# Kernel optimization log

Measured on AMD Instinct MI355X. Metric: run time of the kernel, lower is better.

The kernel has to match this reference:

```python
import jax, jax.numpy as jnp
import numpy as np

DIM_IN = 256  # dim_in_d * dim_in_length


def _quad_feats(h):
    # h: [B, d] -> [B, d + d*(d+1)//2] : concat(h, triu(outer(h, h)))
    d = h.shape[1]
    iu, ju = jnp.triu_indices(d)  # includes diagonal, matching torch.triu_indices
    outer = h[:, :, None] * h[:, None, :]          # [B, d, d]
    hsq = outer[:, iu, ju]                         # [B, d*(d+1)//2]
    return jnp.concatenate([h, hsq], axis=-1)


def setup_inputs() -> dict:
    key = jax.random.key(0)
    ks = jax.random.split(key, 7)
    d = DIM_IN
    q = d + (d * d + d) // 2  # 33152
    scale = 0.01  # keep activations bounded through quadratic features
    return {
        "x": jax.random.normal(ks[0], (4096, 16, 16), dtype=jnp.float32),
        "W0": jax.random.normal(ks[1], (256, q), dtype=jnp.float32) * scale,
        "b0": jax.random.normal(ks[2], (256,), dtype=jnp.float32) * scale,
        "W1": jax.random.normal(ks[3], (256, q), dtype=jnp.float32) * scale,
        "b1": jax.random.normal(ks[4], (256,), dtype=jnp.float32) * scale,
        "W2": jax.random.normal(ks[5], (10, q), dtype=jnp.float32) * scale,
        "b2": jax.random.normal(ks[6], (10,), dtype=jnp.float32) * scale,
    }


def reference(x, W0, b0, W1, b1, W2, b2):
    B = x.shape[0]
    h = x.reshape(B, -1)  # flatten: [B, dim_in_d*dim_in_length]
    for W, b in ((W0, b0), (W1, b1), (W2, b2)):
        z = _quad_feats(h)                  # [B, d + d(d+1)/2]
        h = jnp.einsum('bq,oq->bo', z, W) + b
    return h
```

## Files before the change

kernel.cpp:

```cpp
#include <hip/hip_runtime.h>
#include <stdint.h>

#define Q_IN 33152
#define NTILES 1160
#define TPC 145

typedef _Float16 half8 __attribute__((ext_vector_type(8)));
typedef float floatx4 __attribute__((ext_vector_type(4)));
typedef uint32_t uint4v __attribute__((ext_vector_type(4)));

__global__ void build_tab(uint32_t* tab) {
  int T = blockIdx.x * 256 + threadIdx.x;
  if (T >= NTILES) return;
  int kch = T / TPC, tt = T % TPC;
  int i0, jb;
  if (tt == 0) { i0 = -1; jb = 32 * kch; }
  else {
    int Q = kch * 144 + (tt - 1);
    int grp = Q >> 5, s = Q & 31;
    int g = 0, base = 0;
    for (; g < 8; ++g) { int cnt = 8 - g; if (grp < base + cnt) break; base += cnt; }
    int jt = grp - base;
    i0 = 32 * g + s;
    jb = 32 * (g + jt);
  }
  tab[T] = (((uint32_t)(uint16_t)(short)i0) << 16) | (uint32_t)(uint16_t)jb;
}

__global__ void convert_w(const float* __restrict__ W, _Float16* __restrict__ Wt,
                          const uint32_t* __restrict__ tab, int NTT, int Oreal) {
  int tid = blockIdx.x * 256 + threadIdx.x;
  if (tid >= NTILES * NTT * 64) return;
  int l = tid & 63;
  int nt = (tid >> 6) % NTT;
  int T = tid / (64 * NTT);
  int o = nt * 16 + (l & 15);
  int koff = (l >> 4) * 8;
  half8 v;
#pragma unroll
  for (int t = 0; t < 8; ++t) v[t] = (_Float16)0.f;
  if (o < Oreal) {
    uint32_t e = tab[T];
    int i0 = (short)(e >> 16);
    int jb = (int)(e & 0xFFFFu);
    const float* row = W + (size_t)o * Q_IN;
    if (i0 < 0) {
#pragma unroll
      for (int t = 0; t < 8; ++t) v[t] = (_Float16)row[jb + koff + t];
    } else {
      int qb = 256 + i0 * 256 - (i0 * (i0 - 1)) / 2 - i0;
#pragma unroll
      for (int t = 0; t < 8; ++t) {
        int j = jb + koff + t;
        if (j >= i0) v[t] = (_Float16)row[qb + j];
      }
    }
  }
  *(half8*)(Wt + (size_t)(T * NTT + nt) * 512 + l * 8) = v;
}

__global__ void reduce_h(const float* __restrict__ part, const float* __restrict__ bias,
                         float* __restrict__ h) {
  int t = blockIdx.x * 256 + threadIdx.x;
  float4 acc = *(const float4*)(bias + ((t & 63) << 2));
#pragma unroll
  for (int k = 0; k < 8; ++k) {
    float4 p = *(const float4*)(part + (size_t)k * 1048576 + t * 4);
    acc.x += p.x; acc.y += p.y; acc.z += p.z; acc.w += p.w;
  }
  *(float4*)(h + t * 4) = acc;
}

__global__ void reduce_out(const float* __restrict__ part2, const float* __restrict__ b2,
                           float* __restrict__ out) {
  int t = blockIdx.x * 256 + threadIdx.x;
  if (t >= 40960) return;
  int b = t / 10, o = t - b * 10;
  float acc = b2[o];
#pragma unroll
  for (int k = 0; k < 8; ++k) acc += part2[(size_t)k * 65536 + b * 16 + o];
  out[t] = acc;
}

__device__ inline floatx4 mfma16(half8 a, half8 b, floatx4 c) {
  return __builtin_amdgcn_mfma_f32_16x16x32_f16(a, b, c, 0, 0, 0);
}

__device__ inline half8 splat_mul_lo(half8 a, uint32_t s) {
  uint4v av = __builtin_bit_cast(uint4v, a), r;
#pragma unroll
  for (int k = 0; k < 4; ++k)
    asm("v_pk_mul_f16 %0, %1, %2 op_sel:[0,0] op_sel_hi:[1,0]"
        : "=v"(r[k]) : "v"(av[k]), "v"(s));
  return __builtin_bit_cast(half8, r);
}
__device__ inline half8 splat_mul_hi(half8 a, uint32_t s) {
  uint4v av = __builtin_bit_cast(uint4v, a), r;
#pragma unroll
  for (int k = 0; k < 4; ++k)
    asm("v_pk_mul_f16 %0, %1, %2 op_sel:[0,1] op_sel_hi:[1,1]"
        : "=v"(r[k]) : "v"(av[k]), "v"(s));
  return __builtin_bit_cast(half8, r);
}

__global__ __launch_bounds__(512, 1) void qgemm_main(
    const float* __restrict__ hIn, const _Float16* __restrict__ Wt,
    float* __restrict__ part, const uint32_t* __restrict__ gtab) {
  __shared__ _Float16 hT[128 * 256];

  const int tid = threadIdx.x;
  const int l = tid & 63;
  const int wid = tid >> 6;
  const int wm = wid >> 2;
  const int wn = wid & 3;
  const int kch = blockIdx.x & 7;
  const int rb = blockIdx.x >> 3;
  const int tbase = kch * TPC;

  const char* gb = (const char*)Wt + (size_t)tbase * 16384;
  const char* gq = gb + 16384;
  const uint32_t lo = (uint32_t)(wn * 4096 + l * 16);

  half8 blin[4];
#pragma unroll
  for (int j = 0; j < 4; ++j)
    blin[j] = *(const half8*)(gb + (lo + j * 1024u));

  half8 G0[2][4], G1[2][4];
  auto issueG0 = [&](uint32_t qt) {
#pragma unroll
    for (int t2 = 0; t2 < 2; ++t2)
#pragma unroll
      for (int j = 0; j < 4; ++j)
        G0[t2][j] = *(const half8*)(gq + (lo + (qt + t2) * 16384u + j * 1024u));
  };
  auto issueG1 = [&](uint32_t qt) {
#pragma unroll
    for (int t2 = 0; t2 < 2; ++t2)
#pragma unroll
      for (int j = 0; j < 4; ++j)
        G1[t2][j] = *(const half8*)(gq + (lo + (qt + t2) * 16384u + j * 1024u));
  };
  issueG0(0);
  issueG1(2);

  {
    int r = tid >> 2, sg = tid & 3;
    const float* src = hIn + (size_t)(rb * 128 + r) * 256 + sg * 64;
    char* dst = (char*)hT + r * 512;
    int xo = (r & 7) << 4;
#pragma unroll
    for (int oc = 0; oc < 8; ++oc) {
      float4 f0 = *(const float4*)(src + oc * 8);
      float4 f1 = *(const float4*)(src + oc * 8 + 4);
      half8 hv;
      hv[0] = (_Float16)f0.x; hv[1] = (_Float16)f0.y;
      hv[2] = (_Float16)f0.z; hv[3] = (_Float16)f0.w;
      hv[4] = (_Float16)f1.x; hv[5] = (_Float16)f1.y;
      hv[6] = (_Float16)f1.z; hv[7] = (_Float16)f1.w;
      *(half8*)(dst + ((sg * 128 + oc * 16) ^ xo)) = hv;
    }
  }
  __syncthreads();

  floatx4 acc[4][4];
#pragma unroll
  for (int mt = 0; mt < 4; ++mt)
#pragma unroll
    for (int nt = 0; nt < 4; ++nt)
#pragma unroll
      for (int rg = 0; rg < 4; ++rg) acc[mt][nt][rg] = 0.f;

  int rowb[4];
#pragma unroll
  for (int mt = 0; mt < 4; ++mt)
    rowb[mt] = (wm * 64 + mt * 16 + (l & 15)) * 512;
  const int xorb = (l & 7) << 4;
  const int koffA = (l >> 4) * 16;
  const char* hTb = (const char*)hT;

  half8 a[4];
  uint4v scu[4];
  int prevjb;

  auto loadA = [&](int jb) {
#pragma unroll
    for (int mt = 0; mt < 4; ++mt)
      a[mt] = *(const half8*)(hTb + rowb[mt] + ((jb * 2 + koffA) ^ xorb));
  };
  auto consumeG0 = [&](const int t2, const int s) {
#pragma unroll
    for (int mt = 0; mt < 4; ++mt) {
      uint32_t sd = scu[mt][s >> 1];
      half8 as_ = (s & 1) ? splat_mul_hi(a[mt], sd) : splat_mul_lo(a[mt], sd);
#pragma unroll
      for (int j = 0; j < 4; ++j)
        acc[mt][j] = mfma16(as_, G0[t2][j], acc[mt][j]);
    }
  };
  auto consumeG1 = [&](const int t2, const int s) {
#pragma unroll
    for (int mt = 0; mt < 4; ++mt) {
      uint32_t sd = scu[mt][s >> 1];
      half8 as_ = (s & 1) ? splat_mul_hi(a[mt], sd) : splat_mul_lo(a[mt], sd);
#pragma unroll
      for (int j = 0; j < 4; ++j)
        acc[mt][j] = mfma16(as_, G1[t2][j], acc[mt][j]);
    }
  };

  {
    uint32_t e0 = gtab[tbase];
    int jb = (int)(e0 & 0xFFFFu);
    loadA(jb);
#pragma unroll
    for (int mt = 0; mt < 4; ++mt)
#pragma unroll
      for (int j = 0; j < 4; ++j)
        acc[mt][j] = mfma16(a[mt], blin[j], acc[mt][j]);
    prevjb = jb;
  }

  uint32_t qt = 0;
  for (int blk = 0; blk < 18; ++blk) {
    uint32_t e = gtab[tbase + 1 + blk * 8];
    int i0b = (int)(e >> 16);
    int jb = (int)(e & 0xFFFFu);
#pragma unroll
    for (int mt = 0; mt < 4; ++mt)
      scu[mt] = *(const uint4v*)(hTb + rowb[mt] + ((i0b * 2) ^ xorb));
    if (jb != prevjb) { prevjb = jb; loadA(jb); }

    consumeG0(0, 0); consumeG0(1, 1); issueG0(qt + 4);
    consumeG1(0, 2); consumeG1(1, 3); issueG1(qt + 6);
    consumeG0(0, 4); consumeG0(1, 5); if (blk < 17) issueG0(qt + 8);
    consumeG1(0, 6); consumeG1(1, 7); if (blk < 17) issueG1(qt + 10);
    qt += 8;
  }

  float* op = part + (size_t)kch * 1048576;
#pragma unroll
  for (int mt = 0; mt < 4; ++mt) {
    int rbase = rb * 128 + wm * 64 + mt * 16 + (l >> 4) * 4;
#pragma unroll
    for (int nt = 0; nt < 4; ++nt) {
      int c = wn * 64 + nt * 16 + (l & 15);
#pragma unroll
      for (int rg = 0; rg < 4; ++rg)
        op[(size_t)(rbase + rg) * 256 + c] = acc[mt][nt][rg];
    }
  }
}

__global__ __launch_bounds__(512, 2) void qgemm_small(
    const float* __restrict__ hIn, const _Float16* __restrict__ Wt,
    float* __restrict__ part2, const uint32_t* __restrict__ gtab) {
  __shared__ _Float16 hT[128 * 256];
  const int tid = threadIdx.x;
  const int l = tid & 63;
  const int wid = tid >> 6;
  const int kch = blockIdx.x & 7;
  const int rb = blockIdx.x >> 3;
  const int tbase = kch * TPC;

  {
    int r = tid >> 2, sg = tid & 3;
    const float* src = hIn + (size_t)(rb * 128 + r) * 256 + sg * 64;
    char* dst = (char*)hT + r * 512;
    int xo = (r & 7) << 4;
#pragma unroll
    for (int oc = 0; oc < 8; ++oc) {
      float4 f0 = *(const float4*)(src + oc * 8);
      float4 f1 = *(const float4*)(src + oc * 8 + 4);
      half8 hv;
      hv[0] = (_Float16)f0.x; hv[1] = (_Float16)f0.y;
      hv[2] = (_Float16)f0.z; hv[3] = (_Float16)f0.w;
      hv[4] = (_Float16)f1.x; hv[5] = (_Float16)f1.y;
      hv[6] = (_Float16)f1.z; hv[7] = (_Float16)f1.w;
      *(half8*)(dst + ((sg * 128 + oc * 16) ^ xo)) = hv;
    }
  }
  __syncthreads();

  floatx4 acc;
#pragma unroll
  for (int rg = 0; rg < 4; ++rg) acc[rg] = 0.f;

  const int rowb = (wid * 16 + (l & 15)) * 512;
  const int xorb = (l & 7) << 4;
  const int koffA = (l >> 4) * 16;
  const char* hTb = (const char*)hT;

  half8 a, sc;
  int prevjb;

  {
    uint32_t e0 = gtab[tbase];
    int jb = (int)(e0 & 0xFFFFu);
    a = *(const half8*)(hTb + rowb + ((jb * 2 + koffA) ^ xorb));
    half8 b = *(const half8*)(Wt + (size_t)tbase * 512 + l * 8);
    acc = mfma16(a, b, acc);
    prevjb = jb;
  }

  for (int u8 = 0; u8 < 18; ++u8) {
    uint32_t e = gtab[tbase + 1 + u8 * 8];
    int i0b = (int)(e >> 16);
    int jb = (int)(e & 0xFFFFu);
    const int ttb = tbase + 1 + u8 * 8;
    half8 bq[8];
#pragma unroll
    for (int s = 0; s < 8; ++s)
      bq[s] = *(const half8*)(Wt + (size_t)(ttb + s) * 512 + l * 8);
    if (jb != prevjb) {
      prevjb = jb;
      a = *(const half8*)(hTb + rowb + ((jb * 2 + koffA) ^ xorb));
    }
    sc = *(const half8*)(hTb + rowb + ((i0b * 2) ^ xorb));
#pragma unroll
    for (int s = 0; s < 8; ++s) {
      _Float16 sv = sc[s];
      half8 sb = {sv, sv, sv, sv, sv, sv, sv, sv};
      acc = mfma16(a * sb, bq[s], acc);
    }
  }

  float* op = part2 + (size_t)kch * 65536;
  const int r0 = rb * 128 + wid * 16 + (l >> 4) * 4;
  const int c = l & 15;
#pragma unroll
  for (int rg = 0; rg < 4; ++rg)
    op[(size_t)(r0 + rg) * 16 + c] = acc[rg];
}

extern "C" void kernel_launch(void* const* d_in, const int* in_sizes, int n_in,
                              void* d_out, int out_size, void* d_ws, size_t ws_size,
                              hipStream_t stream) {
  const float* x = (const float*)d_in[0];
  const float* W0 = (const float*)d_in[1];
  const float* b0 = (const float*)d_in[2];
  const float* W1 = (const float*)d_in[3];
  const float* b1 = (const float*)d_in[4];
  const float* W2 = (const float*)d_in[5];
  const float* b2 = (const float*)d_in[6];
  float* out = (float*)d_out;

  char* ws = (char*)d_ws;
  float* h1 = (float*)ws;
  float* h2 = (float*)(ws + (4u << 20));
  _Float16* Wt = (_Float16*)(ws + (8u << 20));
  uint32_t* tab = (uint32_t*)(ws + (8u << 20) + 19005440u);
  float* part = (float*)(ws + (28u << 20));
  float* part2 = part;

  build_tab<<<(NTILES + 255) / 256, 256, 0, stream>>>(tab);

  convert_w<<<(NTILES * 16 * 64) / 256, 256, 0, stream>>>(W0, Wt, tab, 16, 256);
  qgemm_main<<<256, 512, 0, stream>>>(x, Wt, part, tab);
  reduce_h<<<1024, 256, 0, stream>>>(part, b0, h1);
  convert_w<<<(NTILES * 16 * 64) / 256, 256, 0, stream>>>(W1, Wt, tab, 16, 256);
  qgemm_main<<<256, 512, 0, stream>>>(h1, Wt, part, tab);
  reduce_h<<<1024, 256, 0, stream>>>(part, b1, h2);
  convert_w<<<(NTILES * 1 * 64 + 255) / 256, 256, 0, stream>>>(W2, Wt, tab, 1, 10);
  qgemm_small<<<256, 512, 0, stream>>>(h2, Wt, part2, tab);
  reduce_out<<<160, 256, 0, stream>>>(part2, b2, out);
}
```

Measured before the change: 249.1 us.

## Shrink weight prefetch buffers in main GEMM and split-K small GEMM further

In the main quadratic GEMM, the double-buffered weight prefetch drops from two tiles per buffer to one tile per buffer, issued after every consume step, with a peeled final block. This frees registers, possibly enough to raise occupancy or cut spills, but the prefetch distance becomes shorter. The small final-layer GEMM is split over twice as many K chunks (512 blocks instead of 256) to use more CUs, and the output reduction now sums 16 partials instead of 8.

```diff
diff --git a/kernel.cpp b/kernel.cpp
--- a/kernel.cpp
+++ b/kernel.cpp
@@ -78,7 +78,7 @@
   int b = t / 10, o = t - b * 10;
   float acc = b2[o];
 #pragma unroll
-  for (int k = 0; k < 8; ++k) acc += part2[(size_t)k * 65536 + b * 16 + o];
+  for (int k = 0; k < 16; ++k) acc += part2[(size_t)k * 65536 + b * 16 + o];
   out[t] = acc;
 }
 
@@ -126,23 +126,19 @@
   for (int j = 0; j < 4; ++j)
     blin[j] = *(const half8*)(gb + (lo + j * 1024u));
 
-  half8 G0[2][4], G1[2][4];
-  auto issueG0 = [&](uint32_t qt) {
-#pragma unroll
-    for (int t2 = 0; t2 < 2; ++t2)
-#pragma unroll
-      for (int j = 0; j < 4; ++j)
-        G0[t2][j] = *(const half8*)(gq + (lo + (qt + t2) * 16384u + j * 1024u));
-  };
-  auto issueG1 = [&](uint32_t qt) {
-#pragma unroll
-    for (int t2 = 0; t2 < 2; ++t2)
-#pragma unroll
-      for (int j = 0; j < 4; ++j)
-        G1[t2][j] = *(const half8*)(gq + (lo + (qt + t2) * 16384u + j * 1024u));
+  half8 G0[4], G1[4];
+  auto issueG0 = [&](uint32_t t) {
+#pragma unroll
+    for (int j = 0; j < 4; ++j)
+      G0[j] = *(const half8*)(gq + (lo + t * 16384u + j * 1024u));
+  };
+  auto issueG1 = [&](uint32_t t) {
+#pragma unroll
+    for (int j = 0; j < 4; ++j)
+      G1[j] = *(const half8*)(gq + (lo + t * 16384u + j * 1024u));
   };
   issueG0(0);
-  issueG1(2);
+  issueG1(1);
 
   {
     int r = tid >> 2, sg = tid & 3;
@@ -188,24 +184,24 @@
     for (int mt = 0; mt < 4; ++mt)
       a[mt] = *(const half8*)(hTb + rowb[mt] + ((jb * 2 + koffA) ^ xorb));
   };
-  auto consumeG0 = [&](const int t2, const int s) {
+  auto consume0 = [&](const int s) {
 #pragma unroll
     for (int mt = 0; mt < 4; ++mt) {
       uint32_t sd = scu[mt][s >> 1];
       half8 as_ = (s & 1) ? splat_mul_hi(a[mt], sd) : splat_mul_lo(a[mt], sd);
 #pragma unroll
       for (int j = 0; j < 4; ++j)
-        acc[mt][j] = mfma16(as_, G0[t2][j], acc[mt][j]);
-    }
-  };
-  auto consumeG1 = [&](const int t2, const int s) {
+        acc[mt][j] = mfma16(as_, G0[j], acc[mt][j]);
+    }
+  };
+  auto consume1 = [&](const int s) {
 #pragma unroll
     for (int mt = 0; mt < 4; ++mt) {
       uint32_t sd = scu[mt][s >> 1];
       half8 as_ = (s & 1) ? splat_mul_hi(a[mt], sd) : splat_mul_lo(a[mt], sd);
 #pragma unroll
       for (int j = 0; j < 4; ++j)
-        acc[mt][j] = mfma16(as_, G1[t2][j], acc[mt][j]);
+        acc[mt][j] = mfma16(as_, G1[j], acc[mt][j]);
     }
   };
 
@@ -222,7 +218,7 @@
   }
 
   uint32_t qt = 0;
-  for (int blk = 0; blk < 18; ++blk) {
+  for (int blk = 0; blk < 17; ++blk) {
     uint32_t e = gtab[tbase + 1 + blk * 8];
     int i0b = (int)(e >> 16);
     int jb = (int)(e & 0xFFFFu);
@@ -231,11 +227,33 @@
       scu[mt] = *(const uint4v*)(hTb + rowb[mt] + ((i0b * 2) ^ xorb));
     if (jb != prevjb) { prevjb = jb; loadA(jb); }
 
-    consumeG0(0, 0); consumeG0(1, 1); issueG0(qt + 4);
-    consumeG1(0, 2); consumeG1(1, 3); issueG1(qt + 6);
-    consumeG0(0, 4); consumeG0(1, 5); if (blk < 17) issueG0(qt + 8);
-    consumeG1(0, 6); consumeG1(1, 7); if (blk < 17) issueG1(qt + 10);
+    consume0(0); issueG0(qt + 2);
+    consume1(1); issueG1(qt + 3);
+    consume0(2); issueG0(qt + 4);
+    consume1(3); issueG1(qt + 5);
+    consume0(4); issueG0(qt + 6);
+    consume1(5); issueG1(qt + 7);
+    consume0(6); issueG0(qt + 8);
+    consume1(7); issueG1(qt + 9);
     qt += 8;
+  }
+  {
+    uint32_t e = gtab[tbase + 1 + 17 * 8];
+    int i0b = (int)(e >> 16);
+    int jb = (int)(e & 0xFFFFu);
+#pragma unroll
+    for (int mt = 0; mt < 4; ++mt)
+      scu[mt] = *(const uint4v*)(hTb + rowb[mt] + ((i0b * 2) ^ xorb));
+    if (jb != prevjb) { prevjb = jb; loadA(jb); }
+
+    consume0(0); issueG0(138);
+    consume1(1); issueG1(139);
+    consume0(2); issueG0(140);
+    consume1(3); issueG1(141);
+    consume0(4); issueG0(142);
+    consume1(5); issueG1(143);
+    consume0(6);
+    consume1(7);
   }
 
   float* op = part + (size_t)kch * 1048576;
@@ -260,7 +278,9 @@
   const int l = tid & 63;
   const int wid = tid >> 6;
   const int kch = blockIdx.x & 7;
-  const int rb = blockIdx.x >> 3;
+  const int rest = blockIdx.x >> 3;
+  const int wk = rest & 1;
+  const int rb = rest >> 1;
   const int tbase = kch * TPC;
 
   {
@@ -292,9 +312,9 @@
   const char* hTb = (const char*)hT;
 
   half8 a, sc;
-  int prevjb;
-
-  {
+  int prevjb = -1;
+
+  if (wk == 0) {
     uint32_t e0 = gtab[tbase];
     int jb = (int)(e0 & 0xFFFFu);
     a = *(const half8*)(hTb + rowb + ((jb * 2 + koffA) ^ xorb));
@@ -303,7 +323,7 @@
     prevjb = jb;
   }
 
-  for (int u8 = 0; u8 < 18; ++u8) {
+  for (int u8 = wk * 9; u8 < wk * 9 + 9; ++u8) {
     uint32_t e = gtab[tbase + 1 + u8 * 8];
     int i0b = (int)(e >> 16);
     int jb = (int)(e & 0xFFFFu);
@@ -325,7 +345,7 @@
     }
   }
 
-  float* op = part2 + (size_t)kch * 65536;
+  float* op = part2 + (size_t)(kch * 2 + wk) * 65536;
   const int r0 = rb * 128 + wid * 16 + (l >> 4) * 4;
   const int c = l & 15;
 #pragma unroll
@@ -362,6 +382,6 @@
   qgemm_main<<<256, 512, 0, stream>>>(h1, Wt, part, tab);
   reduce_h<<<1024, 256, 0, stream>>>(part, b1, h2);
   convert_w<<<(NTILES * 1 * 64 + 255) / 256, 256, 0, stream>>>(W2, Wt, tab, 1, 10);
-  qgemm_small<<<256, 512, 0, stream>>>(h2, Wt, part2, tab);
+  qgemm_small<<<512, 512, 0, stream>>>(h2, Wt, part2, tab);
   reduce_out<<<160, 256, 0, stream>>>(part2, b2, out);
 }
```

After: 252.7 us. About the same (+1.4%).
